# Performance work log

Hardware: AMD Instinct MI355X
Metric: run time of the kernel (lower is better)

Reference implementation:

```python
import jax, jax.numpy as jnp
import numpy as np

B = 131072          # batch of fermion configurations
S = 256             # sys_size
NUP = 16            # num_fillings[0]
NDOWN = 16          # num_fillings[1]


def _random_occupancy(rng, b, s, nfill):
    # exactly `nfill` ones per row, uniformly random positions
    r = rng.random((b, s))
    perm_rank = np.argsort(r, axis=1).argsort(axis=1)  # a random permutation per row
    return (perm_rank < nfill).astype(np.float32)


def setup_inputs() -> dict:
    rng = np.random.default_rng(0)
    cfg_up = _random_occupancy(rng, B, S, NUP)
    cfg_down = _random_occupancy(rng, B, S, NDOWN)
    config_fermion = jnp.asarray(np.concatenate([cfg_up, cfg_down], axis=1))  # (B, 2S)
    key = jax.random.key(0)
    k1, k2 = jax.random.split(key)
    states_up = jax.random.normal(k1, (S, NUP), dtype=jnp.float32)
    states_down = jax.random.normal(k2, (S, NDOWN), dtype=jnp.float32)
    return {"config_fermion": config_fermion, "states_up": states_up, "states_down": states_down}


def reference(config_fermion, states_up, states_down):
    s = states_up.shape[0]
    nup = states_up.shape[1]
    ndown = states_down.shape[1]
    cfg_up = config_fermion[:, :s]      # (B, S) of {0,1}
    cfg_down = config_fermion[:, s:]
    # indices of occupied sites, ascending (torch.nonzero order); top_k breaks
    # ties by lowest index, then sort ascending
    idx_up = jnp.sort(jax.lax.top_k(cfg_up, nup)[1], axis=1)        # (B, Nup)
    idx_down = jnp.sort(jax.lax.top_k(cfg_down, ndown)[1], axis=1)  # (B, Ndown)
    mats_up = states_up[idx_up]         # (B, Nup, Nup) gather of orbital rows
    mats_down = states_down[idx_down]   # (B, Ndown, Ndown)
    det_up = jnp.linalg.det(mats_up)
    det_down = jnp.linalg.det(mats_down)
    return det_up * det_down
```

## Files before the change

kernel.cpp:

```cpp
#include <hip/hip_runtime.h>

static __device__ __forceinline__ unsigned umax2(unsigned a, unsigned b) { return a > b ? a : b; }

static __device__ __forceinline__ float qb(float v, int sel) {
    int i = __float_as_int(v), r;
    switch (sel) {
        case 0:  r = __builtin_amdgcn_update_dpp(0, i, 0x00, 0xF, 0xF, true); break;
        case 1:  r = __builtin_amdgcn_update_dpp(0, i, 0x55, 0xF, 0xF, true); break;
        case 2:  r = __builtin_amdgcn_update_dpp(0, i, 0xAA, 0xF, 0xF, true); break;
        default: r = __builtin_amdgcn_update_dpp(0, i, 0xFF, 0xF, 0xF, true); break;
    }
    return __int_as_float(r);
}

static __device__ __forceinline__ int mbcnt64(unsigned long long m, int acc) {
    acc = __builtin_amdgcn_mbcnt_lo((unsigned)m, acc);
    acc = __builtin_amdgcn_mbcnt_hi((unsigned)(m >> 32), acc);
    return acc;
}

__global__ __launch_bounds__(256, 4) void slater_det_main(
    const float* __restrict__ cfg,
    const float* __restrict__ sup,
    const float* __restrict__ sdn,
    float* __restrict__ out,
    unsigned* __restrict__ ws_count,
    unsigned* __restrict__ ws_rec,
    unsigned cap)
{
    __shared__ __align__(16) int idx_lds[4][16][16];

    const int tid  = threadIdx.x;
    const int wave = tid >> 6;
    const int lane = tid & 63;
    const int wb0  = (blockIdx.x * 4 + wave) * 8;
    const float* base = cfg + (size_t)wb0 * 512 + (size_t)lane * 4;

    float4 c[8];
#pragma unroll
    for (int d = 0; d < 8; ++d) c[d] = *(const float4*)(base + (size_t)d * 256);
#pragma unroll
    for (int d = 0; d < 16; ++d) {
        float4 v = c[d & 7];
        if (d < 8)
            c[d & 7] = *(const float4*)(base + (size_t)(d + 8) * 256);
        bool n0 = v.x != 0.f, n1 = v.y != 0.f, n2 = v.z != 0.f, n3 = v.w != 0.f;
        unsigned long long b0 = __ballot(n0);
        unsigned long long b1 = __ballot(n1);
        unsigned long long b2 = __ballot(n2);
        unsigned long long b3 = __ballot(n3);
        int r = mbcnt64(b3, mbcnt64(b2, mbcnt64(b1, mbcnt64(b0, 0))));
        int pos = lane * 4;
        if (n0 && r < 16) idx_lds[wave][d][r] = pos;
        r += n0;
        if (n1 && r < 16) idx_lds[wave][d][r] = pos + 1;
        r += n1;
        if (n2 && r < 16) idx_lds[wave][d][r] = pos + 2;
        r += n2;
        if (n3 && r < 16) idx_lds[wave][d][r] = pos + 3;
    }
    asm volatile("s_waitcnt lgkmcnt(0)" ::: "memory");
    __builtin_amdgcn_sched_barrier(0);

    const int g = lane >> 2;
    const int q = lane & 3;
    const int4 ri = *(const int4*)&idx_lds[wave][g][q * 4];
    const float* tab = (g & 1) ? sdn : sup;
    const int rid[4] = {ri.x, ri.y, ri.z, ri.w};

    float rr[4][16];
#pragma unroll
    for (int j = 0; j < 4; ++j) {
        const float* p = tab + (size_t)rid[j] * 16;
        float4 a = *(const float4*)(p + 0);
        float4 b = *(const float4*)(p + 4);
        float4 e = *(const float4*)(p + 8);
        float4 f = *(const float4*)(p + 12);
        rr[j][0]=a.x;  rr[j][1]=a.y;  rr[j][2]=a.z;  rr[j][3]=a.w;
        rr[j][4]=b.x;  rr[j][5]=b.y;  rr[j][6]=b.z;  rr[j][7]=b.w;
        rr[j][8]=e.x;  rr[j][9]=e.y;  rr[j][10]=e.z; rr[j][11]=e.w;
        rr[j][12]=f.x; rr[j][13]=f.y; rr[j][14]=f.z; rr[j][15]=f.w;
    }

    float det = 1.f;
    bool bad = false;
#pragma unroll
    for (int k = 0; k < 16; ++k) {
        const int sel = k >> 2;
        const int jp  = k & 3;
        float piv = qb(rr[jp][k], sel);
        det *= piv;
        bad = bad || (fabsf(piv) < 1e-4f);
        float inv = __builtin_amdgcn_rcpf(piv);
        float f0 = rr[0][k] * inv;
        float f1 = rr[1][k] * inv;
        float f2 = rr[2][k] * inv;
        float f3 = rr[3][k] * inv;
#pragma unroll
        for (int cc = k + 1; cc < 16; ++cc) {
            float pcc = qb(rr[jp][cc], sel);
            rr[0][cc] = __builtin_fmaf(-f0, pcc, rr[0][cc]);
            rr[1][cc] = __builtin_fmaf(-f1, pcc, rr[1][cc]);
            rr[2][cc] = __builtin_fmaf(-f2, pcc, rr[2][cc]);
            rr[3][cc] = __builtin_fmaf(-f3, pcc, rr[3][cc]);
        }
    }

    int badflag = bad ? 1 : 0;
    int partnerbad = __shfl_xor(badflag, 4);
    if ((badflag | partnerbad) && (lane & 7) == 0) {
        unsigned slot = atomicAdd(ws_count, 1u);
        if (slot < cap) {
            unsigned* rec = ws_rec + slot * 12;
            rec[0] = (unsigned)(wb0 + (lane >> 3));
            const int gU = lane >> 2;
#pragma unroll
            for (int t = 0; t < 4; ++t) {
                const int* iu = &idx_lds[wave][gU][t * 4];
                const int* id = &idx_lds[wave][gU | 1][t * 4];
                rec[1 + t] = (unsigned)iu[0] | ((unsigned)iu[1] << 8)
                           | ((unsigned)iu[2] << 16) | ((unsigned)iu[3] << 24);
                rec[5 + t] = (unsigned)id[0] | ((unsigned)id[1] << 8)
                           | ((unsigned)id[2] << 16) | ((unsigned)id[3] << 24);
            }
        }
    }

    float prod = det * __shfl_xor(det, 4);
    if ((lane & 7) == 0) out[wb0 + (lane >> 3)] = prod;
}

__global__ __launch_bounds__(256) void slater_det_cleanup(
    const float* __restrict__ sup,
    const float* __restrict__ sdn,
    float* __restrict__ out,
    const unsigned* __restrict__ ws_count,
    const unsigned* __restrict__ ws_rec,
    unsigned cap)
{
    unsigned n = *ws_count;
    if (n > cap) n = cap;
    const int tid  = blockIdx.x * 256 + threadIdx.x;
    const int unit = tid >> 3;
    const int nunits = (int)(gridDim.x * 256) >> 3;
    const int l8   = threadIdx.x & 7;
    const int wl   = threadIdx.x & 63;
    const int q    = wl & 3;
    const int gbase = wl & ~3;

    for (unsigned item = unit; item < n; item += nunits) {
        const unsigned* rec = ws_rec + item * 12;
        const unsigned batch = rec[0];
        const int half = l8 >> 2;
        const unsigned pk = rec[1 + half * 4 + q];
        const int rid[4] = { (int)(pk & 255u), (int)((pk >> 8) & 255u),
                             (int)((pk >> 16) & 255u), (int)(pk >> 24) };
        const float* tab = half ? sdn : sup;

        float rr[4][16];
#pragma unroll
        for (int j = 0; j < 4; ++j) {
            const float* p = tab + (size_t)rid[j] * 16;
            float4 a = *(const float4*)(p + 0);
            float4 b = *(const float4*)(p + 4);
            float4 e = *(const float4*)(p + 8);
            float4 f = *(const float4*)(p + 12);
            rr[j][0]=a.x;  rr[j][1]=a.y;  rr[j][2]=a.z;  rr[j][3]=a.w;
            rr[j][4]=b.x;  rr[j][5]=b.y;  rr[j][6]=b.z;  rr[j][7]=b.w;
            rr[j][8]=e.x;  rr[j][9]=e.y;  rr[j][10]=e.z; rr[j][11]=e.w;
            rr[j][12]=f.x; rr[j][13]=f.y; rr[j][14]=f.z; rr[j][15]=f.w;
        }

        unsigned am = 0xFu;
        float fdet = 1.f;
        int flips = 0;
#pragma unroll
        for (int k = 0; k < 16; ++k) {
            unsigned a0 = (__float_as_uint(rr[0][k]) & 0x7FFFFFF0u) | (unsigned)(q*4+0);
            unsigned a1 = (__float_as_uint(rr[1][k]) & 0x7FFFFFF0u) | (unsigned)(q*4+1);
            unsigned a2 = (__float_as_uint(rr[2][k]) & 0x7FFFFFF0u) | (unsigned)(q*4+2);
            unsigned a3 = (__float_as_uint(rr[3][k]) & 0x7FFFFFF0u) | (unsigned)(q*4+3);
            unsigned key0 = (am & 1u) ? a0 : (unsigned)(q*4+0);
            unsigned key1 = (am & 2u) ? a1 : (unsigned)(q*4+1);
            unsigned key2 = (am & 4u) ? a2 : (unsigned)(q*4+2);
            unsigned key3 = (am & 8u) ? a3 : (unsigned)(q*4+3);
            unsigned kloc = umax2(umax2(key0, key1), umax2(key2, key3));
            int jloc = (int)(kloc & 3u);
            float crow[16];
#pragma unroll
            for (int cc = k; cc < 16; ++cc) {
                float t01 = (jloc & 1) ? rr[1][cc] : rr[0][cc];
                float t23 = (jloc & 1) ? rr[3][cc] : rr[2][cc];
                crow[cc] = (jloc & 2) ? t23 : t01;
            }
            unsigned ko = kloc;
            ko = umax2(ko, (unsigned)__shfl_xor((int)ko, 1));
            ko = umax2(ko, (unsigned)__shfl_xor((int)ko, 2));
            int p   = (int)(ko & 15u);
            int src = gbase | (p >> 2);
            float prow[16];
#pragma unroll
            for (int cc = k; cc < 16; ++cc) prow[cc] = __shfl(crow[cc], src);
            float piv = prow[k];
            fdet *= piv;
            int t = p - q * 4;
            unsigned mlt = (t <= 0) ? 0u : ((t >= 4) ? 0xFu : ((1u << t) - 1u));
            int cnt = __popc(am & mlt);
            cnt += __shfl_xor(cnt, 1);
            cnt += __shfl_xor(cnt, 2);
            flips += cnt;
            if (q == (p >> 2)) am &= ~(1u << (p & 3));
            float inv = 1.0f / piv;
            float f0 = rr[0][k] * inv;
            float f1 = rr[1][k] * inv;
            float f2 = rr[2][k] * inv;
            float f3 = rr[3][k] * inv;
#pragma unroll
            for (int cc = k + 1; cc < 16; ++cc) {
                rr[0][cc] = __builtin_fmaf(-f0, prow[cc], rr[0][cc]);
                rr[1][cc] = __builtin_fmaf(-f1, prow[cc], rr[1][cc]);
                rr[2][cc] = __builtin_fmaf(-f2, prow[cc], rr[2][cc]);
                rr[3][cc] = __builtin_fmaf(-f3, prow[cc], rr[3][cc]);
            }
        }
        float det = (flips & 1) ? -fdet : fdet;
        float prod = det * __shfl_xor(det, 4);
        if (l8 == 0) out[batch] = prod;
    }
}

extern "C" void kernel_launch(void* const* d_in, const int* in_sizes, int n_in,
                              void* d_out, int out_size, void* d_ws, size_t ws_size,
                              hipStream_t stream) {
    const float* cfg = (const float*)d_in[0];
    const float* sup = (const float*)d_in[1];
    const float* sdn = (const float*)d_in[2];
    float* outp = (float*)d_out;
    unsigned* ws_count = (unsigned*)d_ws;
    unsigned* ws_rec   = (unsigned*)d_ws + 4;
    unsigned cap = (unsigned)((ws_size - 16) / 48);
    const int B = in_sizes[0] / 512;
    const int blocks = B / 32;

    hipMemsetAsync(d_ws, 0, 16, stream);
    slater_det_main<<<blocks, 256, 0, stream>>>(cfg, sup, sdn, outp,
                                                ws_count, ws_rec, cap);
    slater_det_cleanup<<<16, 256, 0, stream>>>(sup, sdn, outp,
                                               ws_count, ws_rec, cap);
}
```

Before: 73.05 us.

## Split index extraction into separate rank kernel writing byte indices to workspace

Moves the ballot-based occupied-site extraction out of the determinant kernel into a dedicated streaming kernel. That kernel writes 8-bit row indices to a workspace buffer. The determinant kernel and the cleanup kernel then read these packed indices, and fallback records shrink to a single batch id. The aim is to separate the bandwidth-bound config scan from the compute-bound elimination so each can run at its own occupancy. In exchange it adds an extra launch and a round trip of the index buffer through global memory.

```diff
diff --git a/kernel.cpp b/kernel.cpp
--- a/kernel.cpp
+++ b/kernel.cpp
@@ -1,6 +1,12 @@
 #include <hip/hip_runtime.h>
 
 static __device__ __forceinline__ unsigned umax2(unsigned a, unsigned b) { return a > b ? a : b; }
+
+static __device__ __forceinline__ int mbcnt64(unsigned long long m, int acc) {
+    acc = __builtin_amdgcn_mbcnt_lo((unsigned)m, acc);
+    acc = __builtin_amdgcn_mbcnt_hi((unsigned)(m >> 32), acc);
+    return acc;
+}
 
 static __device__ __forceinline__ float qb(float v, int sel) {
     int i = __float_as_int(v), r;
@@ -13,14 +19,45 @@
     return __int_as_float(r);
 }
 
-static __device__ __forceinline__ int mbcnt64(unsigned long long m, int acc) {
-    acc = __builtin_amdgcn_mbcnt_lo((unsigned)m, acc);
-    acc = __builtin_amdgcn_mbcnt_hi((unsigned)(m >> 32), acc);
-    return acc;
-}
-
-__global__ __launch_bounds__(256, 4) void slater_det_main(
+__global__ __launch_bounds__(256) void rank_kernel(
     const float* __restrict__ cfg,
+    unsigned char* __restrict__ idx,
+    int nhalves)
+{
+    const int lane = threadIdx.x & 63;
+    const int wid  = (int)((blockIdx.x * blockDim.x + threadIdx.x) >> 6);
+    const int nw   = (int)((gridDim.x * blockDim.x) >> 6);
+
+    for (int h0 = wid * 4; h0 < nhalves; h0 += nw * 4) {
+        float4 v[4];
+#pragma unroll
+        for (int u = 0; u < 4; ++u)
+            v[u] = *(const float4*)(cfg + (size_t)(h0 + u) * 256 + (size_t)lane * 4);
+#pragma unroll
+        for (int u = 0; u < 4; ++u) {
+            const int h = h0 + u;
+            bool n0 = v[u].x != 0.f, n1 = v[u].y != 0.f,
+                 n2 = v[u].z != 0.f, n3 = v[u].w != 0.f;
+            unsigned long long b0 = __ballot(n0);
+            unsigned long long b1 = __ballot(n1);
+            unsigned long long b2 = __ballot(n2);
+            unsigned long long b3 = __ballot(n3);
+            int r = mbcnt64(b3, mbcnt64(b2, mbcnt64(b1, mbcnt64(b0, 0))));
+            unsigned char* o = idx + (size_t)h * 16;
+            unsigned char pos = (unsigned char)(lane * 4);
+            if (n0 && r < 16) o[r] = pos;
+            r += n0;
+            if (n1 && r < 16) o[r] = pos + 1;
+            r += n1;
+            if (n2 && r < 16) o[r] = pos + 2;
+            r += n2;
+            if (n3 && r < 16) o[r] = pos + 3;
+        }
+    }
+}
+
+__global__ __launch_bounds__(256) void det_kernel(
+    const unsigned char* __restrict__ idx,
     const float* __restrict__ sup,
     const float* __restrict__ sdn,
     float* __restrict__ out,
@@ -28,45 +65,15 @@
     unsigned* __restrict__ ws_rec,
     unsigned cap)
 {
-    __shared__ __align__(16) int idx_lds[4][16][16];
-
     const int tid  = threadIdx.x;
     const int wave = tid >> 6;
     const int lane = tid & 63;
     const int wb0  = (blockIdx.x * 4 + wave) * 8;
-    const float* base = cfg + (size_t)wb0 * 512 + (size_t)lane * 4;
-
-    float4 c[8];
-#pragma unroll
-    for (int d = 0; d < 8; ++d) c[d] = *(const float4*)(base + (size_t)d * 256);
-#pragma unroll
-    for (int d = 0; d < 16; ++d) {
-        float4 v = c[d & 7];
-        if (d < 8)
-            c[d & 7] = *(const float4*)(base + (size_t)(d + 8) * 256);
-        bool n0 = v.x != 0.f, n1 = v.y != 0.f, n2 = v.z != 0.f, n3 = v.w != 0.f;
-        unsigned long long b0 = __ballot(n0);
-        unsigned long long b1 = __ballot(n1);
-        unsigned long long b2 = __ballot(n2);
-        unsigned long long b3 = __ballot(n3);
-        int r = mbcnt64(b3, mbcnt64(b2, mbcnt64(b1, mbcnt64(b0, 0))));
-        int pos = lane * 4;
-        if (n0 && r < 16) idx_lds[wave][d][r] = pos;
-        r += n0;
-        if (n1 && r < 16) idx_lds[wave][d][r] = pos + 1;
-        r += n1;
-        if (n2 && r < 16) idx_lds[wave][d][r] = pos + 2;
-        r += n2;
-        if (n3 && r < 16) idx_lds[wave][d][r] = pos + 3;
-    }
-    asm volatile("s_waitcnt lgkmcnt(0)" ::: "memory");
-    __builtin_amdgcn_sched_barrier(0);
-
     const int g = lane >> 2;
-    const int q = lane & 3;
-    const int4 ri = *(const int4*)&idx_lds[wave][g][q * 4];
     const float* tab = (g & 1) ? sdn : sup;
-    const int rid[4] = {ri.x, ri.y, ri.z, ri.w};
+
+    uchar4 pk = *(const uchar4*)(idx + (size_t)wb0 * 32 + (size_t)lane * 4);
+    const int rid[4] = {pk.x, pk.y, pk.z, pk.w};
 
     float rr[4][16];
 #pragma unroll
@@ -110,27 +117,15 @@
     int partnerbad = __shfl_xor(badflag, 4);
     if ((badflag | partnerbad) && (lane & 7) == 0) {
         unsigned slot = atomicAdd(ws_count, 1u);
-        if (slot < cap) {
-            unsigned* rec = ws_rec + slot * 12;
-            rec[0] = (unsigned)(wb0 + (lane >> 3));
-            const int gU = lane >> 2;
-#pragma unroll
-            for (int t = 0; t < 4; ++t) {
-                const int* iu = &idx_lds[wave][gU][t * 4];
-                const int* id = &idx_lds[wave][gU | 1][t * 4];
-                rec[1 + t] = (unsigned)iu[0] | ((unsigned)iu[1] << 8)
-                           | ((unsigned)iu[2] << 16) | ((unsigned)iu[3] << 24);
-                rec[5 + t] = (unsigned)id[0] | ((unsigned)id[1] << 8)
-                           | ((unsigned)id[2] << 16) | ((unsigned)id[3] << 24);
-            }
-        }
+        if (slot < cap) ws_rec[slot] = (unsigned)(wb0 + (lane >> 3));
     }
 
     float prod = det * __shfl_xor(det, 4);
     if ((lane & 7) == 0) out[wb0 + (lane >> 3)] = prod;
 }
 
-__global__ __launch_bounds__(256) void slater_det_cleanup(
+__global__ __launch_bounds__(256) void cleanup_kernel(
+    const unsigned char* __restrict__ idx,
     const float* __restrict__ sup,
     const float* __restrict__ sdn,
     float* __restrict__ out,
@@ -149,13 +144,10 @@
     const int gbase = wl & ~3;
 
     for (unsigned item = unit; item < n; item += nunits) {
-        const unsigned* rec = ws_rec + item * 12;
-        const unsigned batch = rec[0];
-        const int half = l8 >> 2;
-        const unsigned pk = rec[1 + half * 4 + q];
-        const int rid[4] = { (int)(pk & 255u), (int)((pk >> 8) & 255u),
-                             (int)((pk >> 16) & 255u), (int)(pk >> 24) };
-        const float* tab = half ? sdn : sup;
+        const unsigned batch = ws_rec[item];
+        uchar4 pk = *(const uchar4*)(idx + (size_t)batch * 32 + (size_t)l8 * 4);
+        const int rid[4] = {pk.x, pk.y, pk.z, pk.w};
+        const float* tab = (l8 >> 2) ? sdn : sup;
 
         float rr[4][16];
 #pragma unroll
@@ -236,15 +228,17 @@
     const float* sup = (const float*)d_in[1];
     const float* sdn = (const float*)d_in[2];
     float* outp = (float*)d_out;
+    const int B = in_sizes[0] / 512;
+
     unsigned* ws_count = (unsigned*)d_ws;
-    unsigned* ws_rec   = (unsigned*)d_ws + 4;
-    unsigned cap = (unsigned)((ws_size - 16) / 48);
-    const int B = in_sizes[0] / 512;
-    const int blocks = B / 32;
+    unsigned char* idxbuf = (unsigned char*)d_ws + 16;
+    unsigned* ws_rec = (unsigned*)((char*)d_ws + 16 + (size_t)B * 32);
+    unsigned cap = (unsigned)((ws_size - 16 - (size_t)B * 32) / 4);
 
     hipMemsetAsync(d_ws, 0, 16, stream);
-    slater_det_main<<<blocks, 256, 0, stream>>>(cfg, sup, sdn, outp,
-                                                ws_count, ws_rec, cap);
-    slater_det_cleanup<<<16, 256, 0, stream>>>(sup, sdn, outp,
-                                               ws_count, ws_rec, cap);
-}
+    rank_kernel<<<2048, 256, 0, stream>>>(cfg, idxbuf, B * 2);
+    det_kernel<<<B / 32, 256, 0, stream>>>(idxbuf, sup, sdn, outp,
+                                           ws_count, ws_rec, cap);
+    cleanup_kernel<<<16, 256, 0, stream>>>(idxbuf, sup, sdn, outp,
+                                           ws_count, ws_rec, cap);
+}
```

After: 85.91 us. 1.18x slower.
